# Kernel optimization log

Measured on AMD Instinct MI355X. Metric: run time of the kernel, lower is better.

Reference implementation:

```python
import jax, jax.numpy as jnp
import numpy as np

BATCH, SEQ_LEN, ENC_IN = 64, 1536, 7
D_MODEL, N_HEADS, D_FF, E_LAYERS = 256, 8, 1024, 2
K_MA, FACTOR = 25, 1
EPS = 1e-5


def setup_inputs() -> dict:
    key = jax.random.key(0)
    ks = jax.random.split(key, 16)
    s = 0.02
    f32 = jnp.float32
    inp = {
        "x_enc": jax.random.normal(ks[0], (BATCH, SEQ_LEN, ENC_IN), f32),
        "emb_w": jax.random.normal(ks[1], (D_MODEL, ENC_IN, 3), f32) * s,
        "Wq": jax.random.normal(ks[2], (E_LAYERS, D_MODEL, D_MODEL), f32) * s,
        "bq": jnp.zeros((E_LAYERS, D_MODEL), f32),
        "Wk": jax.random.normal(ks[3], (E_LAYERS, D_MODEL, D_MODEL), f32) * s,
        "bk": jnp.zeros((E_LAYERS, D_MODEL), f32),
        "Wv": jax.random.normal(ks[4], (E_LAYERS, D_MODEL, D_MODEL), f32) * s,
        "bv": jnp.zeros((E_LAYERS, D_MODEL), f32),
        "Wo": jax.random.normal(ks[5], (E_LAYERS, D_MODEL, D_MODEL), f32) * s,
        "bo": jnp.zeros((E_LAYERS, D_MODEL), f32),
        "Wc1": jax.random.normal(ks[6], (E_LAYERS, D_FF, D_MODEL), f32) * s,
        "bc1": jnp.zeros((E_LAYERS, D_FF), f32),
        "Wc2": jax.random.normal(ks[7], (E_LAYERS, D_MODEL, D_FF), f32) * s,
        "bc2": jnp.zeros((E_LAYERS, D_MODEL), f32),
        "ln_w": jnp.ones((D_MODEL,), f32),
        "ln_b": jnp.zeros((D_MODEL,), f32),
        "proj_w": jax.random.normal(ks[8], (176, 2 * D_MODEL), f32) * s,
        "proj_b": jnp.zeros((176,), f32),
    }
    return inp


def _moving_avg(x, k):
    # x: [B,L,D]; replicate-pad (k-1)//2 both ends, mean filter size k (stride 1)
    p = (k - 1) // 2
    xp = jnp.concatenate([jnp.repeat(x[:, :1], p, axis=1), x,
                          jnp.repeat(x[:, -1:], p, axis=1)], axis=1)
    cs = jnp.cumsum(xp, axis=1)
    cs = jnp.concatenate([jnp.zeros_like(cs[:, :1]), cs], axis=1)
    return (cs[:, k:] - cs[:, :-k]) / k


def _decomp(x):
    mm = _moving_avg(x, K_MA)
    return x - mm, mm


def _autocorrelation(q, k, v):
    # q,k,v: [B,L,H,E] -> [B,L,H,E]
    B, L, H, E = q.shape
    qf = jnp.fft.rfft(jnp.transpose(q, (0, 2, 3, 1)), axis=-1)
    kf = jnp.fft.rfft(jnp.transpose(k, (0, 2, 3, 1)), axis=-1)
    corr = jnp.fft.irfft(qf * jnp.conj(kf), n=L, axis=-1)   # [B,H,E,L]
    vals = jnp.transpose(v, (0, 2, 3, 1))                    # [B,H,E,L]
    top_k = int(FACTOR * np.log(L))
    mean_corr = corr.mean(axis=(1, 2))                       # [B,L]
    weights, delay = jax.lax.top_k(mean_corr, top_k)         # [B,top_k]
    tmp_corr = jax.nn.softmax(weights, axis=-1)
    idx0 = jnp.arange(L)
    agg = jnp.zeros_like(vals)
    for i in range(top_k):                                    # small fixed count (7)
        idx = (idx0[None, :] + delay[:, i, None]) % L         # [B,L] circular delay
        pat = jnp.take_along_axis(vals, jnp.broadcast_to(idx[:, None, None, :], vals.shape), axis=-1)
        agg = agg + pat * tmp_corr[:, i, None, None, None]
    return jnp.transpose(agg, (0, 3, 1, 2))


def _attn_layer(x, Wq, bq, Wk, bk, Wv, bv, Wo, bo):
    B, L, _ = x.shape
    E = D_MODEL // N_HEADS
    q = (x @ Wq.T + bq).reshape(B, L, N_HEADS, E)
    k = (x @ Wk.T + bk).reshape(B, L, N_HEADS, E)
    v = (x @ Wv.T + bv).reshape(B, L, N_HEADS, E)
    out = _autocorrelation(q, k, v).reshape(B, L, D_MODEL)
    return out @ Wo.T + bo


def reference(x_enc, emb_w, Wq, bq, Wk, bk, Wv, bv, Wo, bo, Wc1, bc1, Wc2, bc2, ln_w, ln_b, proj_w, proj_b):
    # token embedding: circular-padded Conv1d(enc_in -> d_model, kernel 3, no bias)
    xp = jnp.concatenate([x_enc[:, -1:], x_enc, x_enc[:, :1]], axis=1)
    x = (jnp.einsum('blc,dc->bld', xp[:, :-2], emb_w[:, :, 0])
         + jnp.einsum('blc,dc->bld', xp[:, 1:-1], emb_w[:, :, 1])
         + jnp.einsum('blc,dc->bld', xp[:, 2:], emb_w[:, :, 2]))
    for l in range(E_LAYERS):
        a = _attn_layer(x, Wq[l], bq[l], Wk[l], bk[l], Wv[l], bv[l], Wo[l], bo[l])
        x, _ = _decomp(x + a)
        y = jax.nn.gelu(jnp.einsum('bld,fd->blf', x, Wc1[l]) + bc1[l], approximate=False)
        y = jnp.einsum('blf,df->bld', y, Wc2[l]) + bc2[l]
        x, _ = _decomp(x + y)
    # my_Layernorm: LN then subtract seq-mean
    mu = x.mean(-1, keepdims=True)
    var = ((x - mu) ** 2).mean(-1, keepdims=True)
    xh = (x - mu) / jnp.sqrt(var + EPS) * ln_w + ln_b
    x = xh - xh.mean(axis=1, keepdims=True)
    out = jnp.concatenate([x.mean(axis=1), x.max(axis=1)], axis=-1)  # [B, 2*d_model]
    out = jax.nn.gelu(out, approximate=False)
    return out @ proj_w.T + proj_b
```

## Files before the change

### kernel.cpp

```cpp
#include <hip/hip_runtime.h>
#include <math.h>

typedef _Float16 half_t;
typedef _Float16 half4 __attribute__((ext_vector_type(4)));
typedef _Float16 half8 __attribute__((ext_vector_type(8)));
typedef short short8 __attribute__((ext_vector_type(8)));
typedef float f32x4 __attribute__((ext_vector_type(4)));
typedef unsigned short u16;
typedef unsigned short u16x4 __attribute__((ext_vector_type(4)));

#define L_SEQ 1536
#define GRAM_PLANE (64*1536)

__device__ __forceinline__ u16 f2bf(float f){
  unsigned u = __float_as_uint(f);
  return (u16)((u + 0x7FFFu + ((u>>16)&1u)) >> 16);
}
__device__ __forceinline__ float bf2f(u16 h){ return __uint_as_float(((unsigned)h)<<16); }
__device__ __forceinline__ float gelu_f(float x){ return 0.5f*x*(1.f+erff(x*0.70710678118f)); }

__device__ __forceinline__ void load_lds16(const void* g, void* l){
  __builtin_amdgcn_global_load_lds((const __attribute__((address_space(1))) void*)g,
                                   (__attribute__((address_space(3))) void*)l, 16, 0, 0);
}
__device__ __forceinline__ f32x4 mfma_bf(short8 a, short8 b, f32x4 c){
  return __builtin_amdgcn_mfma_f32_16x16x32_bf16(a,b,c,0,0,0);
}
__device__ __forceinline__ f32x4 mfma_fp(half8 a, half8 b, f32x4 c){
  return __builtin_amdgcn_mfma_f32_16x16x32_f16(a,b,c,0,0,0);
}

__device__ __forceinline__ void store_pair(float v, size_t row, int d, u16* X2B){
  size_t r2 = row*512 + d;
  u16 hi = f2bf(v);
  X2B[r2] = hi;
  X2B[r2+256] = f2bf(v - bf2f(hi));
}

__global__ __launch_bounds__(256) void w4b_k(const float* __restrict__ W, u16* __restrict__ W4, int n){
  int i = blockIdx.x*256 + threadIdx.x;
  if (i >= n) return;
  int ro = i >> 8, c = i & 255;
  float v = W[i];
  u16 hi = f2bf(v);
  u16 lo = f2bf(v - bf2f(hi));
  u16* r = W4 + (size_t)ro*1024;
  r[c] = hi; r[c+256] = hi; r[c+512] = lo; r[c+768] = lo;
}
__global__ __launch_bounds__(256) void castb_k(const float* __restrict__ W, u16* __restrict__ Wb, int n){
  for (int i = blockIdx.x*256 + threadIdx.x; i < n; i += gridDim.x*256)
    Wb[i] = f2bf(W[i]);
}

__global__ __launch_bounds__(256) void embed_k(const float* __restrict__ XE, const float* __restrict__ EW,
                                               u16* __restrict__ X2B){
  __shared__ float xs[66*7];
  int b = blockIdx.x / 24, lc = blockIdx.x % 24;
  int l0 = lc*64;
  int tid = threadIdx.x;
  for (int i = tid; i < 66*7; i += 256){
    int r = i/7, c = i%7;
    int g = l0 - 1 + r; if (g < 0) g += L_SEQ; if (g >= L_SEQ) g -= L_SEQ;
    xs[i] = XE[((size_t)b*L_SEQ + g)*7 + c];
  }
  __syncthreads();
  int d = tid;
  float wp[21];
  #pragma unroll
  for (int i=0;i<21;i++) wp[i] = EW[d*21+i];
  for (int j = 0; j < 64; j++){
    float acc = 0.f;
    #pragma unroll
    for (int c = 0; c < 7; c++)
      #pragma unroll
      for (int k = 0; k < 3; k++) acc += xs[(j+k)*7+c] * wp[c*3+k];
    store_pair(acc, (size_t)b*L_SEQ + l0 + j, d, X2B);
  }
}

template<int EPI, bool KMOD>
__global__ __launch_bounds__(256) void gemm_k(const u16* __restrict__ A, int lda,
                                              const u16* __restrict__ B, int ldb,
                                              const float* __restrict__ bias,
                                              void* __restrict__ C, int ldc,
                                              const u16* __restrict__ res,
                                              int K){
  __shared__ __align__(16) u16 As[2][128*32];
  __shared__ __align__(16) u16 Bs[2][128*32];
  const int tid = threadIdx.x;
  const int wv = tid>>6, ln = tid&63;
  const int lrow = ln&15, lk = ln>>4;
  const int bm = blockIdx.x, bn = blockIdx.y;
  const int wr = wv>>1, wc = wv&1;
  f32x4 acc[4][4];
  #pragma unroll
  for (int i=0;i<4;i++)
    #pragma unroll
    for (int j=0;j<4;j++) acc[i][j] = f32x4{0.f,0.f,0.f,0.f};

  const int nt = K >> 5;
  auto stage = [&](int buf, int t){
    int k0 = t*32;
    int ka = KMOD ? (k0 & 511) : k0;
    #pragma unroll
    for (int p=0;p<2;p++){
      int chunk = (wv*2+p)*64 + ln;
      int row = chunk>>2, c16 = chunk&3;
      int sw = (row>>1)&3;
      load_lds16(A + (size_t)(bm*128 + row)*lda + (ka + ((c16^sw)*8)), &As[buf][(size_t)chunk*8]);
      load_lds16(B + (size_t)(bn*128 + row)*ldb + (k0 + ((c16^sw)*8)), &Bs[buf][(size_t)chunk*8]);
    }
  };

  stage(0, 0);
  int cur = 0;
  const int swR = (lrow>>1)&3;
  for (int t = 0; t < nt; t++){
    __syncthreads();
    if (t+1 < nt) stage(cur^1, t+1);
    short8 av[4], bv[4];
    #pragma unroll
    for (int mi=0;mi<4;mi++) av[mi] = *(const short8*)&As[cur][(wr*64 + mi*16 + lrow)*32 + ((lk^swR)*8)];
    #pragma unroll
    for (int ni=0;ni<4;ni++) bv[ni] = *(const short8*)&Bs[cur][(wc*64 + ni*16 + lrow)*32 + ((lk^swR)*8)];
    #pragma unroll
    for (int mi=0;mi<4;mi++)
      #pragma unroll
      for (int ni=0;ni<4;ni++)
        acc[mi][ni] = mfma_bf(av[mi], bv[ni], acc[mi][ni]);
    cur ^= 1;
  }

  #pragma unroll
  for (int mi=0;mi<4;mi++){
    #pragma unroll
    for (int ni=0;ni<4;ni++){
      int col = bn*128 + wc*64 + ni*16 + lrow;
      float bs = bias[col];
      #pragma unroll
      for (int r=0;r<4;r++){
        int row = bm*128 + wr*64 + mi*16 + lk*4 + r;
        float v = acc[mi][ni][r] + bs;
        if (EPI==0){ ((u16*)C)[(size_t)row*ldc + col] = f2bf(v); }
        else if (EPI==1){ ((u16*)C)[(size_t)row*ldc + col] = f2bf(gelu_f(v)); }
        else {
          float rv = bf2f(res[(size_t)row*512 + col]) + bf2f(res[(size_t)row*512 + 256 + col]);
          ((float*)C)[(size_t)row*ldc + col] = v + rv;
        }
      }
    }
  }
}

__global__ __launch_bounds__(256) void gemmqkv_k(const u16* __restrict__ A,
                                                 const u16* __restrict__ B,
                                                 const float* __restrict__ bq,
                                                 const float* __restrict__ bk,
                                                 const float* __restrict__ bv,
                                                 u16* __restrict__ Q2, u16* __restrict__ K2,
                                                 u16* __restrict__ V2){
  __shared__ __align__(16) u16 As[2][128*32];
  __shared__ __align__(16) u16 Bs[2][128*32];
  const int tid = threadIdx.x;
  const int wv = tid>>6, ln = tid&63;
  const int lrow = ln&15, lk = ln>>4;
  const int bm = blockIdx.x, bn = blockIdx.y;
  const int wr = wv>>1, wc = wv&1;
  f32x4 acc[4][4];
  #pragma unroll
  for (int i=0;i<4;i++)
    #pragma unroll
    for (int j=0;j<4;j++) acc[i][j] = f32x4{0.f,0.f,0.f,0.f};

  auto stage = [&](int buf, int t){
    int k0 = t*32;
    int ka = k0 & 511;
    #pragma unroll
    for (int p=0;p<2;p++){
      int chunk = (wv*2+p)*64 + ln;
      int row = chunk>>2, c16 = chunk&3;
      int sw = (row>>1)&3;
      load_lds16(A + (size_t)(bm*128 + row)*512 + (ka + ((c16^sw)*8)), &As[buf][(size_t)chunk*8]);
      load_lds16(B + (size_t)(bn*128 + row)*1024 + (k0 + ((c16^sw)*8)), &Bs[buf][(size_t)chunk*8]);
    }
  };

  stage(0, 0);
  int cur = 0;
  const int swR = (lrow>>1)&3;
  for (int t = 0; t < 32; t++){
    __syncthreads();
    if (t+1 < 32) stage(cur^1, t+1);
    short8 av[4], bv_[4];
    #pragma unroll
    for (int mi=0;mi<4;mi++) av[mi] = *(const short8*)&As[cur][(wr*64 + mi*16 + lrow)*32 + ((lk^swR)*8)];
    #pragma unroll
    for (int ni=0;ni<4;ni++) bv_[ni] = *(const short8*)&Bs[cur][(wc*64 + ni*16 + lrow)*32 + ((lk^swR)*8)];
    #pragma unroll
    for (int mi=0;mi<4;mi++)
      #pragma unroll
      for (int ni=0;ni<4;ni++)
        acc[mi][ni] = mfma_bf(av[mi], bv_[ni], acc[mi][ni]);
    cur ^= 1;
  }

  const int proj = bn>>1, half = bn&1;
  const float* bias = (proj==0) ? bq : (proj==1) ? bk : bv;
  #pragma unroll
  for (int mi=0;mi<4;mi++){
    #pragma unroll
    for (int ni=0;ni<4;ni++){
      int col = half*128 + wc*64 + ni*16 + lrow;
      float bs = bias[col];
      #pragma unroll
      for (int r=0;r<4;r++){
        int row = bm*128 + wr*64 + mi*16 + lk*4 + r;
        float v = acc[mi][ni][r] + bs;
        if (proj==2){
          V2[(size_t)row*256 + col] = f2bf(v);
        } else {
          half_t hi = (half_t)v;
          half_t* Cp = (half_t*)((proj==0) ? Q2 : K2);
          Cp[(size_t)row*512 + col] = hi;
          Cp[(size_t)row*512 + 256 + col] = (half_t)((v - (float)hi)*512.f);
        }
      }
    }
  }
}

__global__ __launch_bounds__(256) void gram_k(const u16* __restrict__ Q2, const u16* __restrict__ K2,
                                              float* __restrict__ MCP){
  __shared__ __align__(16) union UN {
    struct { u16 As[2][256*32]; u16 Bs[2][64*32]; } s;
    float C[64][65];
  } u;
  const int tid = threadIdx.x, wv = tid>>6, ln = tid&63;
  const int lrow = ln&15, lk = ln>>4;
  int id = blockIdx.x;
  int low = id & 7, hi = id >> 3;
  int half = hi & 1;
  int tb = (hi>>1) & 7;
  int b  = ((hi >> 4) << 3) | low;
  const size_t base = (size_t)b*L_SEQ*512;
  f32x4 acc[4][4];
  #pragma unroll
  for (int i=0;i<4;i++)
    #pragma unroll
    for (int j=0;j<4;j++) acc[i][j] = f32x4{0.f,0.f,0.f,0.f};

  auto stageG = [&](int buf, int it){
    int jt = half*12 + (it>>3), dt = it&7;
    int t0 = tb*192 + jt*64, d0 = dt*32;
    #pragma unroll
    for (int p=0;p<4;p++){
      int chunk = (p*4+wv)*64 + ln;
      int row = chunk>>2, c16 = chunk&3;
      int sw = (row>>1)&3;
      int g = t0 + row; if (g >= L_SEQ) g -= L_SEQ;
      load_lds16(Q2 + base + (size_t)g*512 + d0 + ((c16^sw)*8), &u.s.As[buf][(size_t)chunk*8]);
    }
    { int chunk = wv*64 + ln;
      int row = chunk>>2, c16 = chunk&3;
      int sw = (row>>1)&3;
      load_lds16(K2 + base + (size_t)(jt*64+row)*512 + d0 + ((c16^sw)*8), &u.s.Bs[buf][(size_t)chunk*8]); }
  };

  stageG(0, 0);
  int cur = 0;
  const int swR = (lrow>>1)&3;
  for (int it = 0; it < 96; it++){
    __syncthreads();
    if (it+1 < 96) stageG(cur^1, it+1);
    half8 av[4], bv[4];
    #pragma unroll
    for (int mi=0;mi<4;mi++) av[mi] = *(const half8*)&u.s.As[cur][(wv*64 + mi*16 + lrow)*32 + ((lk^swR)*8)];
    #pragma unroll
    for (int ni=0;ni<4;ni++) bv[ni] = *(const half8*)&u.s.Bs[cur][(ni*16 + lrow)*32 + ((lk^swR)*8)];
    #pragma unroll
    for (int mi=0;mi<4;mi++)
      #pragma unroll
      for (int ni=0;ni<4;ni++)
        acc[mi][ni] = mfma_fp(av[mi], bv[ni], acc[mi][ni]);
    cur ^= 1;
  }
  __syncthreads();

  float dsum = 0.f;
  for (int r = 0; r < 4; r++){
    if (wv == r){
      #pragma unroll
      for (int mi=0;mi<4;mi++)
        #pragma unroll
        for (int ni=0;ni<4;ni++)
          #pragma unroll
          for (int rr=0;rr<4;rr++)
            u.C[mi*16 + lk*4 + rr][ni*16 + lrow] = acc[mi][ni][rr];
    }
    __syncthreads();
    if (tid < 192){
      int jlo = r*64 - tid;      if (jlo < 0) jlo = 0;
      int jhi = r*64 + 64 - tid; if (jhi > 64) jhi = 64;
      for (int j = jlo; j < jhi; j++) dsum += u.C[tid + j - r*64][j];
    }
    __syncthreads();
  }
  if (tid < 192) MCP[(size_t)half*GRAM_PLANE + (size_t)b*L_SEQ + tb*192 + tid] = dsum * (1.f/256.f);
}

__global__ __launch_bounds__(256) void topk_k(const float* __restrict__ MCP, int* __restrict__ CANDI,
                                              int* __restrict__ NCAND){
  __shared__ float v[1536];
  __shared__ float rv[256]; __shared__ int ri[256];
  __shared__ float sred[256];
  __shared__ float s_margin;
  __shared__ float topv[16]; __shared__ int topi[16];
  int b = blockIdx.x, tid = threadIdx.x;
  const float* r0 = MCP + (size_t)b*L_SEQ;
  const float* r1 = MCP + GRAM_PLANE + (size_t)b*L_SEQ;
  float s = 0.f, ss = 0.f;
  for (int j=0;j<6;j++){
    int idx = tid+256*j;
    float x = r0[idx] + r1[idx];
    v[idx] = x; s += x; ss += x*x;
  }
  sred[tid]=s; __syncthreads();
  for (int o=128;o>0;o>>=1){ if (tid<o) sred[tid]+=sred[tid+o]; __syncthreads(); }
  float mean = sred[0]*(1.f/1536.f); __syncthreads();
  sred[tid]=ss; __syncthreads();
  for (int o=128;o>0;o>>=1){ if (tid<o) sred[tid]+=sred[tid+o]; __syncthreads(); }
  if (tid==0){
    float var = sred[0]*(1.f/1536.f) - mean*mean; if (var < 0.f) var = 0.f;
    s_margin = 0.02f*sqrtf(var) + 1e-8f;
  }
  __syncthreads();
  for (int it = 0; it < 16; it++){
    float bv_ = -3.4e38f; int bi_ = 1<<30;
    for (int j=0;j<6;j++){ int idx = tid+256*j; float x = v[idx];
      if (x > bv_ || (x == bv_ && idx < bi_)){ bv_ = x; bi_ = idx; } }
    rv[tid]=bv_; ri[tid]=bi_; __syncthreads();
    for (int o=128;o>0;o>>=1){
      if (tid<o){
        float xo = rv[tid+o]; int io = ri[tid+o];
        if (xo > rv[tid] || (xo == rv[tid] && io < ri[tid])){ rv[tid]=xo; ri[tid]=io; }
      }
      __syncthreads();
    }
    if (tid==0){ topv[it]=rv[0]; topi[it]=ri[0]; v[ri[0]] = -3.4e38f; }
    __syncthreads();
  }
  if (tid==0){
    float thr = topv[6] - s_margin;
    int nc = 7; while (nc < 16 && topv[nc] >= thr) nc++;
    NCAND[b] = nc;
    for (int i=0;i<16;i++) CANDI[b*16+i] = topi[i];
  }
}

__global__ __launch_bounds__(256) void recompute3_k(const u16* __restrict__ Q2, const u16* __restrict__ K2,
                                                    const int* __restrict__ CANDI, const int* __restrict__ NCAND,
                                                    float* __restrict__ CANDV){
  int id = blockIdx.x;
  int low = id & 7, hi = id >> 3;
  int ci = hi & 15;
  int b = (hi >> 4)*8 + low;
  if (ci >= NCAND[b]) return;
  int tau = CANDI[b*16+ci];
  const half_t* qb = (const half_t*)Q2 + (size_t)b*L_SEQ*512;
  const half_t* kb = (const half_t*)K2 + (size_t)b*L_SEQ*512;
  int tid = threadIdx.x, wv = tid>>6, ln = tid&63;
  int d0 = ln*4;
  float acc = 0.f;
  #pragma unroll 4
  for (int t = wv; t < L_SEQ; t += 4){
    int g = t + tau; if (g >= L_SEQ) g -= L_SEQ;
    half4 qh = *(const half4*)(qb + (size_t)g*512 + d0);
    half4 ql = *(const half4*)(qb + (size_t)g*512 + 256 + d0);
    half4 kh = *(const half4*)(kb + (size_t)t*512 + d0);
    half4 kl = *(const half4*)(kb + (size_t)t*512 + 256 + d0);
    #pragma unroll
    for (int j=0;j<4;j++){
      float qv = (float)qh[j] + (float)ql[j]*(1.f/512.f);
      float kv = (float)kh[j] + (float)kl[j]*(1.f/512.f);
      acc += qv*kv;
    }
  }
  #pragma unroll
  for (int o=32;o>0;o>>=1) acc += __shfl_xor(acc,o);
  __shared__ float w4[4];
  if (ln==0) w4[wv]=acc;
  __syncthreads();
  if (tid==0) CANDV[b*16+ci] = (w4[0]+w4[1]+w4[2]+w4[3])*(1.f/256.f);
}

__global__ void select7_k(const int* __restrict__ CANDI, const float* __restrict__ CANDV,
                          const int* __restrict__ NCAND, int* __restrict__ DLY, float* __restrict__ WGT){
  int b = blockIdx.x;
  if (threadIdx.x != 0) return;
  int nc = NCAND[b];
  float vals[16]; int idx[16];
  #pragma unroll
  for (int i=0;i<16;i++){ vals[i] = (i<nc)? CANDV[b*16+i] : -3.4e38f; idx[i] = CANDI[b*16+i]; }
  for (int i=0;i<7;i++){
    int best=i;
    for (int j=i+1;j<16;j++)
      if (vals[j]>vals[best] || (vals[j]==vals[best] && idx[j]<idx[best])) best=j;
    float tv=vals[i]; vals[i]=vals[best]; vals[best]=tv;
    int ti=idx[i]; idx[i]=idx[best]; idx[best]=ti;
  }
  float m=vals[0], e[7], sum=0.f;
  #pragma unroll
  for (int i=0;i<7;i++){ e[i]=expf(vals[i]-m); sum+=e[i]; }
  #pragma unroll
  for (int i=0;i<7;i++){ WGT[b*8+i]=e[i]/sum; DLY[b*8+i]=idx[i]; }
}

__global__ __launch_bounds__(256) void agg_k(const u16* __restrict__ V, const int* __restrict__ DLY,
                                             const float* __restrict__ WGT, u16* __restrict__ AGG){
  int gid = blockIdx.x*256 + threadIdx.x;
  int b = gid / 49152;
  int rem = gid % 49152;
  int t = rem >> 5, du = rem & 31;
  float w[7]; int dl[7];
  #pragma unroll
  for (int i=0;i<7;i++){ w[i]=WGT[b*8+i]; dl[i]=DLY[b*8+i]; }
  float a[8] = {0,0,0,0,0,0,0,0};
  #pragma unroll
  for (int i=0;i<7;i++){
    int g = t + dl[i]; if (g >= L_SEQ) g -= L_SEQ;
    short8 hv = *(const short8*)(V + ((size_t)b*L_SEQ + g)*256 + du*8);
    #pragma unroll
    for (int j=0;j<8;j++) a[j] += w[i]*bf2f((u16)hv[j]);
  }
  short8 o;
  #pragma unroll
  for (int j=0;j<8;j++) o[j] = (short)f2bf(a[j]);
  *(short8*)(AGG + ((size_t)b*L_SEQ + t)*256 + du*8) = o;
}

__global__ __launch_bounds__(256) void decomp_k(const float* __restrict__ S, u16* __restrict__ X2B){
  int b = blockIdx.y, lc = blockIdx.x, d = threadIdx.x;
  const float* s = S + (size_t)b*L_SEQ*256;
  int l0 = lc*128;
  float w = 0.f;
  for (int j=-12;j<=12;j++){
    int g = l0+j; if (g < 0) g = 0; if (g > L_SEQ-1) g = L_SEQ-1;
    w += s[(size_t)g*256+d];
  }
  for (int l = l0; l < l0+128; l++){
    float c = s[(size_t)l*256+d];
    store_pair(c - w*(1.f/25.f), (size_t)b*L_SEQ + l, d, X2B);
    int ga = l+13; if (ga > L_SEQ-1) ga = L_SEQ-1;
    int gb = l-12; if (gb < 0) gb = 0;
    w += s[(size_t)ga*256+d] - s[(size_t)gb*256+d];
  }
}

__global__ __launch_bounds__(256) void lncr_k(const u16* __restrict__ X2B, const float* __restrict__ LW,
                                              const float* __restrict__ LB, float* __restrict__ RS,
                                              float* __restrict__ RM){
  int b = blockIdx.y, lc = blockIdx.x;
  int tid = threadIdx.x, wv = tid>>6, l_ = tid&63;
  f32x4 lw = *(const f32x4*)(LW + l_*4);
  f32x4 lb = *(const f32x4*)(LB + l_*4);
  float cs[4] = {0,0,0,0};
  float cm[4] = {-3.4e38f,-3.4e38f,-3.4e38f,-3.4e38f};
  size_t tok0 = (size_t)b*L_SEQ + lc*128 + wv*32;
  for (int it = 0; it < 32; it++){
    const u16* xr = X2B + (tok0+it)*512 + l_*4;
    u16x4 hi = *(const u16x4*)xr;
    u16x4 lo = *(const u16x4*)(xr+256);
    float v[4]; float s=0.f, ss=0.f;
    #pragma unroll
    for (int j=0;j<4;j++){ v[j] = bf2f(hi[j]) + bf2f(lo[j]); s += v[j]; ss += v[j]*v[j]; }
    #pragma unroll
    for (int o=32;o>0;o>>=1){ s += __shfl_xor(s,o); ss += __shfl_xor(ss,o); }
    float mean = s*(1.f/256.f);
    float var = ss*(1.f/256.f) - mean*mean;
    float rstd = rsqrtf(var + 1e-5f);
    #pragma unroll
    for (int j=0;j<4;j++){
      float xh = (v[j]-mean)*rstd*lw[j] + lb[j];
      cs[j] += xh; cm[j] = fmaxf(cm[j], xh);
    }
  }
  __shared__ float S[4][256];
  __shared__ float M[4][256];
  #pragma unroll
  for (int j=0;j<4;j++){ S[wv][l_*4+j] = cs[j]; M[wv][l_*4+j] = cm[j]; }
  __syncthreads();
  float s4 = S[0][tid]+S[1][tid]+S[2][tid]+S[3][tid];
  float m4 = fmaxf(fmaxf(M[0][tid],M[1][tid]), fmaxf(M[2][tid],M[3][tid]));
  RS[((size_t)b*12+lc)*256+tid] = s4;
  RM[((size_t)b*12+lc)*256+tid] = m4;
}

__global__ __launch_bounds__(256) void final_k(const float* __restrict__ RS, const float* __restrict__ RM,
                                               const float* __restrict__ PW, const float* __restrict__ PB,
                                               float* __restrict__ OUT){
  __shared__ float feat[256];
  int b = blockIdx.x, tid = threadIdx.x;
  float s = 0.f, m = -3.4e38f;
  for (int c=0;c<12;c++){
    s += RS[((size_t)b*12+c)*256+tid];
    m = fmaxf(m, RM[((size_t)b*12+c)*256+tid]);
  }
  float mu = s*(1.f/1536.f);
  feat[tid] = gelu_f(m - mu);
  __syncthreads();
  if (tid < 176){
    float acc = PB[tid];
    for (int d=0; d<256; d++) acc += feat[d]*PW[(size_t)tid*512 + 256 + d];
    OUT[(size_t)b*176 + tid] = acc;
  }
}

extern "C" void kernel_launch(void* const* d_in, const int* in_sizes, int n_in,
                              void* d_out, int out_size, void* d_ws, size_t ws_size,
                              hipStream_t stream){
  const float* x_enc=(const float*)d_in[0];
  const float* emb_w=(const float*)d_in[1];
  const float* Wq=(const float*)d_in[2];  const float* bq=(const float*)d_in[3];
  const float* Wk=(const float*)d_in[4];  const float* bk=(const float*)d_in[5];
  const float* Wv=(const float*)d_in[6];  const float* bv=(const float*)d_in[7];
  const float* Wo=(const float*)d_in[8];  const float* bo=(const float*)d_in[9];
  const float* Wc1=(const float*)d_in[10]; const float* bc1=(const float*)d_in[11];
  const float* Wc2=(const float*)d_in[12]; const float* bc2=(const float*)d_in[13];
  const float* ln_w=(const float*)d_in[14]; const float* ln_b=(const float*)d_in[15];
  const float* pw=(const float*)d_in[16];  const float* pb=(const float*)d_in[17];
  (void)in_sizes; (void)n_in; (void)out_size;

  int G = 1;
  while (G < 8){
    size_t need = (size_t)40*1024*1024 + (7ull*(size_t)(98304/G)*1024ull)/2;
    if (need <= ws_size) break;
    G *= 2;
  }
  const int NBG = 64 / G;
  const int NT  = NBG * L_SEQ;

  char* ws = (char*)d_ws;
  size_t off = 0;
  auto alloc = [&](size_t bytes)->void*{
    void* p = ws + off; off += (bytes + 255) & ~(size_t)255; return p;
  };
  u16* W4QKV = (u16*)alloc((size_t)2*768*1024*2);
  u16* WOb  = (u16*)alloc((size_t)2*256*256*2);
  u16* WC1b = (u16*)alloc((size_t)2*1024*256*2);
  u16* WC2b = (u16*)alloc((size_t)2*256*1024*2);
  float* MCP = (float*)alloc((size_t)2*GRAM_PLANE*4);
  int*  CANDI=(int*)  alloc(64*16*4);
  float*CANDV=(float*)alloc(64*16*4);
  int*  NCAND=(int*)  alloc(64*4);
  int*  DLY = (int*)  alloc(64*8*4);
  float*WGT = (float*)alloc(64*8*4);
  float*RS  = (float*)alloc((size_t)64*12*256*4);
  float*RM  = (float*)alloc((size_t)64*12*256*4);
  u16* X2B = (u16*)alloc((size_t)NT*512*2);
  u16* Q2  = (u16*)alloc((size_t)NT*512*2);
  u16* K2  = (u16*)alloc((size_t)NT*512*2);
  u16* V2  = (u16*)alloc((size_t)NT*256*2);

  float* SUM = (float*)K2;
  u16*   AGG = Q2;
  u16*   HH  = Q2;

  for (int l = 0; l < 2; l++){
    w4b_k<<<256,256,0,stream>>>(Wq + (size_t)l*65536, W4QKV + ((size_t)l*768+  0)*1024, 65536);
    w4b_k<<<256,256,0,stream>>>(Wk + (size_t)l*65536, W4QKV + ((size_t)l*768+256)*1024, 65536);
    w4b_k<<<256,256,0,stream>>>(Wv + (size_t)l*65536, W4QKV + ((size_t)l*768+512)*1024, 65536);
  }
  castb_k<<<512,256,0,stream>>>(Wo, WOb, 2*256*256);
  castb_k<<<2048,256,0,stream>>>(Wc1, WC1b, 2*1024*256);
  castb_k<<<2048,256,0,stream>>>(Wc2, WC2b, 2*256*1024);

  for (int g = 0; g < G; g++){
    const float* xe = x_enc + (size_t)g*NBG*L_SEQ*7;
    float* outg = (float*)d_out + (size_t)g*NBG*176;

    embed_k<<<NT/64,256,0,stream>>>(xe, emb_w, X2B);

    for (int l = 0; l < 2; l++){
      gemmqkv_k<<<dim3(NT/128,6),256,0,stream>>>(X2B, W4QKV+(size_t)l*768*1024,
                                                 bq+l*256, bk+l*256, bv+l*256, Q2, K2, V2);
      gram_k<<<NBG*16,256,0,stream>>>(Q2, K2, MCP);
      topk_k<<<NBG,256,0,stream>>>(MCP, CANDI, NCAND);
      recompute3_k<<<NBG*16,256,0,stream>>>(Q2, K2, CANDI, NCAND, CANDV);
      select7_k<<<NBG,64,0,stream>>>(CANDI, CANDV, NCAND, DLY, WGT);
      agg_k<<<NT/8,256,0,stream>>>(V2, DLY, WGT, AGG);
      gemm_k<2,false><<<dim3(NT/128,2),256,0,stream>>>(AGG,256, WOb+(size_t)l*65536,256, bo+l*256, SUM, 256, X2B, 256);
      decomp_k<<<dim3(12,NBG),256,0,stream>>>(SUM, X2B);
      for (int c = 0; c < 2; c++){
        const u16* Ac = X2B + (size_t)c*(NT/2)*512;
        gemm_k<1,false><<<dim3(NT/256,8),256,0,stream>>>(Ac,512, WC1b+(size_t)l*262144,256, bc1+l*1024, HH, 1024, nullptr, 256);
        gemm_k<2,false><<<dim3(NT/256,2),256,0,stream>>>(HH,1024, WC2b+(size_t)l*262144,1024, bc2+l*256,
                                                         SUM+(size_t)c*(NT/2)*256, 256, X2B+(size_t)c*(NT/2)*512, 1024);
      }
      decomp_k<<<dim3(12,NBG),256,0,stream>>>(SUM, X2B);
    }

    lncr_k<<<dim3(12,NBG),256,0,stream>>>(X2B, ln_w, ln_b, RS, RM);
    final_k<<<NBG,256,0,stream>>>(RS, RM, pw, pb, outg);
  }
}
```

Before: 2.424 ms.

## Store residual sums as bf16 hi/lo pairs and swap GEMM grid axes

The residual-sum GEMM epilogue now writes a pair of bf16 values (hi and lo remainder) instead of fp32, and decomp_k reads and adds that pair. Both layouts take the same bytes, but the SUM buffer now matches the X2B split-bf16 layout used elsewhere. The GEMM grids are also transposed so blockIdx.x walks the N tiles, which groups blocks sharing the same A rows for better L2 reuse. The split pair keeps roughly fp32 precision, though with a small rounding difference.

```diff
diff --git a/kernel.cpp b/kernel.cpp
--- a/kernel.cpp
+++ b/kernel.cpp
@@ -90,7 +90,7 @@
   const int tid = threadIdx.x;
   const int wv = tid>>6, ln = tid&63;
   const int lrow = ln&15, lk = ln>>4;
-  const int bm = blockIdx.x, bn = blockIdx.y;
+  const int bm = blockIdx.y, bn = blockIdx.x;
   const int wr = wv>>1, wc = wv&1;
   f32x4 acc[4][4];
   #pragma unroll
@@ -145,7 +145,10 @@
         else if (EPI==1){ ((u16*)C)[(size_t)row*ldc + col] = f2bf(gelu_f(v)); }
         else {
           float rv = bf2f(res[(size_t)row*512 + col]) + bf2f(res[(size_t)row*512 + 256 + col]);
-          ((float*)C)[(size_t)row*ldc + col] = v + rv;
+          float s = v + rv;
+          u16 hi = f2bf(s);
+          ((u16*)C)[(size_t)row*512 + col] = hi;
+          ((u16*)C)[(size_t)row*512 + 256 + col] = f2bf(s - bf2f(hi));
         }
       }
     }
@@ -164,7 +167,7 @@
   const int tid = threadIdx.x;
   const int wv = tid>>6, ln = tid&63;
   const int lrow = ln&15, lk = ln>>4;
-  const int bm = blockIdx.x, bn = blockIdx.y;
+  const int bm = blockIdx.y, bn = blockIdx.x;
   const int wr = wv>>1, wc = wv&1;
   f32x4 acc[4][4];
   #pragma unroll
@@ -438,21 +441,25 @@
   *(short8*)(AGG + ((size_t)b*L_SEQ + t)*256 + du*8) = o;
 }
 
-__global__ __launch_bounds__(256) void decomp_k(const float* __restrict__ S, u16* __restrict__ X2B){
+__global__ __launch_bounds__(256) void decomp_k(const u16* __restrict__ SP, u16* __restrict__ X2B){
   int b = blockIdx.y, lc = blockIdx.x, d = threadIdx.x;
-  const float* s = S + (size_t)b*L_SEQ*256;
+  const u16* s = SP + (size_t)b*L_SEQ*512;
+  auto rd = [&](int l)->float{
+    size_t o = (size_t)l*512 + d;
+    return bf2f(s[o]) + bf2f(s[o+256]);
+  };
   int l0 = lc*128;
   float w = 0.f;
   for (int j=-12;j<=12;j++){
     int g = l0+j; if (g < 0) g = 0; if (g > L_SEQ-1) g = L_SEQ-1;
-    w += s[(size_t)g*256+d];
+    w += rd(g);
   }
   for (int l = l0; l < l0+128; l++){
-    float c = s[(size_t)l*256+d];
+    float c = rd(l);
     store_pair(c - w*(1.f/25.f), (size_t)b*L_SEQ + l, d, X2B);
     int ga = l+13; if (ga > L_SEQ-1) ga = L_SEQ-1;
     int gb = l-12; if (gb < 0) gb = 0;
-    w += s[(size_t)ga*256+d] - s[(size_t)gb*256+d];
+    w += rd(ga) - rd(gb);
   }
 }
 
@@ -561,9 +568,9 @@
   u16* K2  = (u16*)alloc((size_t)NT*512*2);
   u16* V2  = (u16*)alloc((size_t)NT*256*2);
 
-  float* SUM = (float*)K2;
-  u16*   AGG = Q2;
-  u16*   HH  = Q2;
+  u16* SUMP = K2;
+  u16* AGG  = Q2;
+  u16* HH   = Q2;
 
   for (int l = 0; l < 2; l++){
     w4b_k<<<256,256,0,stream>>>(Wq + (size_t)l*65536, W4QKV + ((size_t)l*768+  0)*1024, 65536);
@@ -581,22 +588,22 @@
     embed_k<<<NT/64,256,0,stream>>>(xe, emb_w, X2B);
 
     for (int l = 0; l < 2; l++){
-      gemmqkv_k<<<dim3(NT/128,6),256,0,stream>>>(X2B, W4QKV+(size_t)l*768*1024,
+      gemmqkv_k<<<dim3(6,NT/128),256,0,stream>>>(X2B, W4QKV+(size_t)l*768*1024,
                                                  bq+l*256, bk+l*256, bv+l*256, Q2, K2, V2);
       gram_k<<<NBG*16,256,0,stream>>>(Q2, K2, MCP);
       topk_k<<<NBG,256,0,stream>>>(MCP, CANDI, NCAND);
       recompute3_k<<<NBG*16,256,0,stream>>>(Q2, K2, CANDI, NCAND, CANDV);
       select7_k<<<NBG,64,0,stream>>>(CANDI, CANDV, NCAND, DLY, WGT);
       agg_k<<<NT/8,256,0,stream>>>(V2, DLY, WGT, AGG);
-      gemm_k<2,false><<<dim3(NT/128,2),256,0,stream>>>(AGG,256, WOb+(size_t)l*65536,256, bo+l*256, SUM, 256, X2B, 256);
-      decomp_k<<<dim3(12,NBG),256,0,stream>>>(SUM, X2B);
+      gemm_k<2,false><<<dim3(2,NT/128),256,0,stream>>>(AGG,256, WOb+(size_t)l*65536,256, bo+l*256, SUMP, 512, X2B, 256);
+      decomp_k<<<dim3(12,NBG),256,0,stream>>>(SUMP, X2B);
       for (int c = 0; c < 2; c++){
         const u16* Ac = X2B + (size_t)c*(NT/2)*512;
-        gemm_k<1,false><<<dim3(NT/256,8),256,0,stream>>>(Ac,512, WC1b+(size_t)l*262144,256, bc1+l*1024, HH, 1024, nullptr, 256);
-        gemm_k<2,false><<<dim3(NT/256,2),256,0,stream>>>(HH,1024, WC2b+(size_t)l*262144,1024, bc2+l*256,
-                                                         SUM+(size_t)c*(NT/2)*256, 256, X2B+(size_t)c*(NT/2)*512, 1024);
+        gemm_k<1,false><<<dim3(8,NT/256),256,0,stream>>>(Ac,512, WC1b+(size_t)l*262144,256, bc1+l*1024, HH, 1024, nullptr, 256);
+        gemm_k<2,false><<<dim3(2,NT/256),256,0,stream>>>(HH,1024, WC2b+(size_t)l*262144,1024, bc2+l*256,
+                                                         SUMP+(size_t)c*(NT/2)*512, 512, X2B+(size_t)c*(NT/2)*512, 1024);
       }
-      decomp_k<<<dim3(12,NBG),256,0,stream>>>(SUM, X2B);
+      decomp_k<<<dim3(12,NBG),256,0,stream>>>(SUMP, X2B);
     }
 
     lncr_k<<<dim3(12,NBG),256,0,stream>>>(X2B, ln_w, ln_b, RS, RM);
```

After: 2.552 ms. 1.05x slower.

## Trim QKV split-precision K dimension and batch recompute candidates per block

Applied to the files above, without the earlier changes.

The QKV weight packing drops the redundant lo*lo term so Q/K use a 768-wide K dimension (hi,hi,lo), and V uses only the bf16 hi product (256 K), cutting the GEMM's K loop from 32 to 24 or 8 tiles per column block. Separately, the candidate-lag recompute kernel now evaluates four candidates per block, reusing each loaded K row across them and launching a quarter as many blocks. The V projection loses its split-precision correction, which lowers its accuracy. Reusing K rows raises register use per thread.

```diff
diff --git a/kernel.cpp b/kernel.cpp
--- a/kernel.cpp
+++ b/kernel.cpp
@@ -37,15 +37,20 @@
   X2B[r2+256] = f2bf(v - bf2f(hi));
 }
 
-__global__ __launch_bounds__(256) void w4b_k(const float* __restrict__ W, u16* __restrict__ W4, int n){
+__global__ __launch_bounds__(256) void w4b768_k(const float* __restrict__ W, u16* __restrict__ W4, int n){
   int i = blockIdx.x*256 + threadIdx.x;
   if (i >= n) return;
   int ro = i >> 8, c = i & 255;
   float v = W[i];
   u16 hi = f2bf(v);
   u16 lo = f2bf(v - bf2f(hi));
-  u16* r = W4 + (size_t)ro*1024;
-  r[c] = hi; r[c+256] = hi; r[c+512] = lo; r[c+768] = lo;
+  u16* r = W4 + (size_t)ro*768;
+  r[c] = hi; r[c+256] = hi; r[c+512] = lo;
+}
+__global__ __launch_bounds__(256) void wvpad_k(const float* __restrict__ W, u16* __restrict__ W4, int n){
+  int i = blockIdx.x*256 + threadIdx.x;
+  if (i >= n) return;
+  W4[(size_t)(i>>8)*768 + (i&255)] = f2bf(W[i]);
 }
 __global__ __launch_bounds__(256) void castb_k(const float* __restrict__ W, u16* __restrict__ Wb, int n){
   for (int i = blockIdx.x*256 + threadIdx.x; i < n; i += gridDim.x*256)
@@ -166,6 +171,7 @@
   const int lrow = ln&15, lk = ln>>4;
   const int bm = blockIdx.x, bn = blockIdx.y;
   const int wr = wv>>1, wc = wv&1;
+  const int nt = (bn < 4) ? 24 : 8;
   f32x4 acc[4][4];
   #pragma unroll
   for (int i=0;i<4;i++)
@@ -181,16 +187,16 @@
       int row = chunk>>2, c16 = chunk&3;
       int sw = (row>>1)&3;
       load_lds16(A + (size_t)(bm*128 + row)*512 + (ka + ((c16^sw)*8)), &As[buf][(size_t)chunk*8]);
-      load_lds16(B + (size_t)(bn*128 + row)*1024 + (k0 + ((c16^sw)*8)), &Bs[buf][(size_t)chunk*8]);
+      load_lds16(B + (size_t)(bn*128 + row)*768 + (k0 + ((c16^sw)*8)), &Bs[buf][(size_t)chunk*8]);
     }
   };
 
   stage(0, 0);
   int cur = 0;
   const int swR = (lrow>>1)&3;
-  for (int t = 0; t < 32; t++){
+  for (int t = 0; t < nt; t++){
     __syncthreads();
-    if (t+1 < 32) stage(cur^1, t+1);
+    if (t+1 < nt) stage(cur^1, t+1);
     short8 av[4], bv_[4];
     #pragma unroll
     for (int mi=0;mi<4;mi++) av[mi] = *(const short8*)&As[cur][(wr*64 + mi*16 + lrow)*32 + ((lk^swR)*8)];
@@ -357,40 +363,60 @@
   }
 }
 
-__global__ __launch_bounds__(256) void recompute3_k(const u16* __restrict__ Q2, const u16* __restrict__ K2,
+__global__ __launch_bounds__(256) void recompute4_k(const u16* __restrict__ Q2, const u16* __restrict__ K2,
                                                     const int* __restrict__ CANDI, const int* __restrict__ NCAND,
                                                     float* __restrict__ CANDV){
   int id = blockIdx.x;
   int low = id & 7, hi = id >> 3;
-  int ci = hi & 15;
-  int b = (hi >> 4)*8 + low;
-  if (ci >= NCAND[b]) return;
-  int tau = CANDI[b*16+ci];
+  int cg = hi & 3;
+  int b = ((hi >> 2) << 3) | low;
+  int nc = NCAND[b];
+  int c0 = cg*4;
+  if (c0 >= nc) return;
+  int tau[4];
+  #pragma unroll
+  for (int i=0;i<4;i++){
+    int ci = c0+i; if (ci > 15) ci = 15;
+    tau[i] = CANDI[b*16+ci];
+  }
   const half_t* qb = (const half_t*)Q2 + (size_t)b*L_SEQ*512;
   const half_t* kb = (const half_t*)K2 + (size_t)b*L_SEQ*512;
   int tid = threadIdx.x, wv = tid>>6, ln = tid&63;
   int d0 = ln*4;
-  float acc = 0.f;
-  #pragma unroll 4
+  float acc[4] = {0.f,0.f,0.f,0.f};
+  #pragma unroll 2
   for (int t = wv; t < L_SEQ; t += 4){
-    int g = t + tau; if (g >= L_SEQ) g -= L_SEQ;
-    half4 qh = *(const half4*)(qb + (size_t)g*512 + d0);
-    half4 ql = *(const half4*)(qb + (size_t)g*512 + 256 + d0);
     half4 kh = *(const half4*)(kb + (size_t)t*512 + d0);
     half4 kl = *(const half4*)(kb + (size_t)t*512 + 256 + d0);
-    #pragma unroll
-    for (int j=0;j<4;j++){
-      float qv = (float)qh[j] + (float)ql[j]*(1.f/512.f);
-      float kv = (float)kh[j] + (float)kl[j]*(1.f/512.f);
-      acc += qv*kv;
-    }
-  }
-  #pragma unroll
-  for (int o=32;o>0;o>>=1) acc += __shfl_xor(acc,o);
-  __shared__ float w4[4];
-  if (ln==0) w4[wv]=acc;
+    float kv[4];
+    #pragma unroll
+    for (int j=0;j<4;j++) kv[j] = (float)kh[j] + (float)kl[j]*(1.f/512.f);
+    #pragma unroll
+    for (int i=0;i<4;i++){
+      int g = t + tau[i]; if (g >= L_SEQ) g -= L_SEQ;
+      const half_t* qr = qb + (size_t)g*512 + d0;
+      half4 qh = *(const half4*)qr;
+      half4 ql = *(const half4*)(qr+256);
+      #pragma unroll
+      for (int j=0;j<4;j++)
+        acc[i] += ((float)qh[j] + (float)ql[j]*(1.f/512.f))*kv[j];
+    }
+  }
+  #pragma unroll
+  for (int i=0;i<4;i++)
+    #pragma unroll
+    for (int o=32;o>0;o>>=1) acc[i] += __shfl_xor(acc[i],o);
+  __shared__ float red[4][4];
+  if (ln==0){
+    #pragma unroll
+    for (int i=0;i<4;i++) red[wv][i] = acc[i];
+  }
   __syncthreads();
-  if (tid==0) CANDV[b*16+ci] = (w4[0]+w4[1]+w4[2]+w4[3])*(1.f/256.f);
+  if (tid < 4){
+    int ci = c0 + tid;
+    if (ci < nc)
+      CANDV[b*16+ci] = (red[0][tid]+red[1][tid]+red[2][tid]+red[3][tid])*(1.f/256.f);
+  }
 }
 
 __global__ void select7_k(const int* __restrict__ CANDI, const float* __restrict__ CANDV,
@@ -544,7 +570,7 @@
   auto alloc = [&](size_t bytes)->void*{
     void* p = ws + off; off += (bytes + 255) & ~(size_t)255; return p;
   };
-  u16* W4QKV = (u16*)alloc((size_t)2*768*1024*2);
+  u16* W4QKV = (u16*)alloc((size_t)2*768*768*2);
   u16* WOb  = (u16*)alloc((size_t)2*256*256*2);
   u16* WC1b = (u16*)alloc((size_t)2*1024*256*2);
   u16* WC2b = (u16*)alloc((size_t)2*256*1024*2);
@@ -566,9 +592,9 @@
   u16*   HH  = Q2;
 
   for (int l = 0; l < 2; l++){
-    w4b_k<<<256,256,0,stream>>>(Wq + (size_t)l*65536, W4QKV + ((size_t)l*768+  0)*1024, 65536);
-    w4b_k<<<256,256,0,stream>>>(Wk + (size_t)l*65536, W4QKV + ((size_t)l*768+256)*1024, 65536);
-    w4b_k<<<256,256,0,stream>>>(Wv + (size_t)l*65536, W4QKV + ((size_t)l*768+512)*1024, 65536);
+    w4b768_k<<<256,256,0,stream>>>(Wq + (size_t)l*65536, W4QKV + ((size_t)l*768+  0)*768, 65536);
+    w4b768_k<<<256,256,0,stream>>>(Wk + (size_t)l*65536, W4QKV + ((size_t)l*768+256)*768, 65536);
+    wvpad_k <<<256,256,0,stream>>>(Wv + (size_t)l*65536, W4QKV + ((size_t)l*768+512)*768, 65536);
   }
   castb_k<<<512,256,0,stream>>>(Wo, WOb, 2*256*256);
   castb_k<<<2048,256,0,stream>>>(Wc1, WC1b, 2*1024*256);
@@ -581,11 +607,11 @@
     embed_k<<<NT/64,256,0,stream>>>(xe, emb_w, X2B);
 
     for (int l = 0; l < 2; l++){
-      gemmqkv_k<<<dim3(NT/128,6),256,0,stream>>>(X2B, W4QKV+(size_t)l*768*1024,
+      gemmqkv_k<<<dim3(NT/128,6),256,0,stream>>>(X2B, W4QKV+(size_t)l*768*768,
                                                  bq+l*256, bk+l*256, bv+l*256, Q2, K2, V2);
       gram_k<<<NBG*16,256,0,stream>>>(Q2, K2, MCP);
       topk_k<<<NBG,256,0,stream>>>(MCP, CANDI, NCAND);
-      recompute3_k<<<NBG*16,256,0,stream>>>(Q2, K2, CANDI, NCAND, CANDV);
+      recompute4_k<<<NBG*4,256,0,stream>>>(Q2, K2, CANDI, NCAND, CANDV);
       select7_k<<<NBG,64,0,stream>>>(CANDI, CANDV, NCAND, DLY, WGT);
       agg_k<<<NT/8,256,0,stream>>>(V2, DLY, WGT, AGG);
       gemm_k<2,false><<<dim3(NT/128,2),256,0,stream>>>(AGG,256, WOb+(size_t)l*65536,256, bo+l*256, SUM, 256, X2B, 256);
```

New measurement: 2.591 ms. 6.9% more time.
